# Kernel optimization log

Hardware: AMD Instinct MI355X
Metric: run time of the kernel (lower is better)

## Reference

```python
import jax, jax.numpy as jnp
import numpy as np

IN_FEATURES = 4096
OUT_FEATURES = 11008
GROUP_SIZE = 32
M_TOKENS = 32
Q_MID = 8  # int4 midpoint: dequant = (q - 8) * scale + zero


def setup_inputs() -> dict:
    key = jax.random.key(0)
    k1, k2, k3, k4 = jax.random.split(key, 4)
    n_groups = IN_FEATURES // GROUP_SIZE
    inputs = {
        "input": jax.random.normal(k1, (M_TOKENS, IN_FEATURES), dtype=jnp.float32),
        "weight": jax.random.randint(k2, (OUT_FEATURES, IN_FEATURES), 0, 16, dtype=jnp.int32),
        "scales_and_zeros": jax.random.normal(k3, (n_groups, OUT_FEATURES, 2), dtype=jnp.float32),
        "bias": jax.random.normal(k4, (OUT_FEATURES,), dtype=jnp.float32),
        "group_size": GROUP_SIZE,
    }
    return inputs


def reference(input, weight, scales_and_zeros, bias, group_size):
    out_features, in_features = weight.shape
    n_groups = in_features // group_size
    # scales/zeros per (group, out) -> [out, n_groups]
    scale = scales_and_zeros[..., 0].T  # [out, G]
    zero = scales_and_zeros[..., 1].T   # [out, G]
    # dequantize int4 weight: w = (q - 8) * scale + zero, per group along in_features
    q = weight.astype(jnp.float32).reshape(out_features, n_groups, group_size)
    w_fp = (q - Q_MID) * scale[:, :, None] + zero[:, :, None]  # [out, G, gs]
    w_fp = w_fp.reshape(out_features, in_features)
    # y = x @ W^T + b
    y = jnp.einsum("bi,oi->bo", input, w_fp) + bias
    return y
```

## Files before the change

kernel.cpp:

```cpp
#include <hip/hip_runtime.h>
#include <hip/hip_bf16.h>
#include <stdint.h>

#define M_TOK 32
#define IN_F 4096
#define OUT_F 11008
#define NSPLIT 8
#define KRANGE (IN_F / NSPLIT)
#define NSTEP  (KRANGE / 32)
#define NKK    (IN_F / 32)
#define NBUF   4

typedef __attribute__((ext_vector_type(8))) short bf16x8;
typedef __attribute__((ext_vector_type(4))) float f32x4;

__device__ inline uint32_t pack_bf16(float a, float b) {
    __hip_bfloat16 ha = __float2bfloat16(a);
    __hip_bfloat16 hb = __float2bfloat16(b);
    uint16_t ua = *(uint16_t*)&ha;
    uint16_t ub = *(uint16_t*)&hb;
    return (uint32_t)ua | ((uint32_t)ub << 16);
}

__global__ void init_out_kernel(const float* __restrict__ bias, float* __restrict__ out) {
    int o = blockIdx.x * 256 + threadIdx.x;
    int m = blockIdx.y;
    out[(size_t)m * OUT_F + o] = bias[o];
}

__global__ void prepack_a_kernel(const float* __restrict__ x, uint4* __restrict__ ws4) {
    int u  = blockIdx.x * 256 + threadIdx.x;
    int kk = u >> 6;
    int l  = u & 63;
    int lm = l & 15;
    int lq = l >> 4;
    int kb = kk * 32 + lq * 8;
    #pragma unroll
    for (int j = 0; j < 2; ++j) {
        const float* xp = x + (size_t)(lm + 16 * j) * IN_F + kb;
        union { uint4 q; uint32_t u[4]; } f;
        f.u[0] = pack_bf16(xp[0], xp[1]);
        f.u[1] = pack_bf16(xp[2], xp[3]);
        f.u[2] = pack_bf16(xp[4], xp[5]);
        f.u[3] = pack_bf16(xp[6], xp[7]);
        ws4[(size_t)kk * 128 + j * 64 + l] = f.q;
    }
}

__launch_bounds__(256)
__global__ void qgemm_kernel(const uint4* __restrict__ af,
                             const int* __restrict__ wq,
                             const float* __restrict__ sz,
                             float* __restrict__ out) {
    __shared__ int    lds_w[NBUF][64 * 32];
    __shared__ uint4  lds_a[NSTEP * 128];
    __shared__ float2 lds_s[NSTEP * 64];

    const int bid = blockIdx.x;
    const int ks  = bid & (NSPLIT - 1);
    const int nb  = bid >> 3;
    const int t   = threadIdx.x;
    const int wv  = t >> 6;
    const int l   = t & 63;
    const int lm  = l & 15;
    const int lq  = l >> 4;

    const int row0 = nb * 64;
    const int row  = row0 + wv * 16 + lm;
    const int k0   = ks * KRANGE;

    const int rs    = t >> 3;
    const int cs    = t & 7;
    const int* gw0  = wq + (size_t)(row0 + rs) * IN_F + k0 + ((cs ^ (rs & 7)) * 4);
    const int* gw1  = gw0 + (size_t)32 * IN_F;

#define GLL(src, dst) \
    __builtin_amdgcn_global_load_lds( \
        (const __attribute__((address_space(1))) int*)(src), \
        (__attribute__((address_space(3))) int*)(dst), 16, 0, 0)

#define STAGE(buf, tile) do {                                 \
    GLL(gw0 + (tile) * 32, &lds_w[(buf)][wv * 256]);          \
    GLL(gw1 + (tile) * 32, &lds_w[(buf)][1024 + wv * 256]);   \
} while (0)

#define WAITV(N) do {                                         \
    asm volatile("s_waitcnt vmcnt(" #N ")" ::: "memory");     \
    __builtin_amdgcn_sched_barrier(0);                        \
} while (0)

#define BAR() do {                                            \
    __builtin_amdgcn_s_barrier();                             \
    __builtin_amdgcn_sched_barrier(0);                        \
} while (0)

    const int rloc = wv * 16 + lm;
    const int c0   = rloc * 32 + (((2 * lq)     ^ (rloc & 7)) * 4);
    const int c1   = rloc * 32 + (((2 * lq + 1) ^ (rloc & 7)) * 4);

    {
        const uint4* asrc = af + (size_t)ks * (NSTEP * 128) + t;
        #pragma unroll
        for (int i = 0; i < 8; ++i)
            GLL(asrc + i * 256, &lds_a[i * 256 + wv * 64]);
    }
    {
        const float* szsrc = sz + ((size_t)(k0 >> 5) * OUT_F + row0) * 2
                                + (size_t)(t >> 5) * OUT_F * 2 + (t & 31) * 4;
        GLL(szsrc,                        &lds_s[wv * 128]);
        GLL(szsrc + (size_t)8 * OUT_F * 2, &lds_s[512 + wv * 128]);
    }
    STAGE(0, 0);
    STAGE(1, 1);
    STAGE(2, 2);
    __builtin_amdgcn_sched_barrier(0);

    f32x4 acc0 = {0.f, 0.f, 0.f, 0.f};
    f32x4 acc1 = {0.f, 0.f, 0.f, 0.f};

#define STEP_BODY(cb, st) do {                                                  \
    int4   q0 = *(const int4*)(&lds_w[(cb)][c0]);                               \
    int4   q1 = *(const int4*)(&lds_w[(cb)][c1]);                               \
    union { uint4 q; bf16x8 v; } a0, a1;                                        \
    a0.q = lds_a[(st) * 128 + l];                                               \
    a1.q = lds_a[(st) * 128 + 64 + l];                                          \
    float2 sv = lds_s[(st) * 64 + rloc];                                        \
    const float sc = sv.x;                                                      \
    const float zp = sv.y - 8.0f * sv.x;                                        \
    union { bf16x8 v; uint32_t u[4]; } bf;                                      \
    bf.u[0] = pack_bf16((float)q0.x * sc + zp, (float)q0.y * sc + zp);          \
    bf.u[1] = pack_bf16((float)q0.z * sc + zp, (float)q0.w * sc + zp);          \
    bf.u[2] = pack_bf16((float)q1.x * sc + zp, (float)q1.y * sc + zp);          \
    bf.u[3] = pack_bf16((float)q1.z * sc + zp, (float)q1.w * sc + zp);          \
    acc0 = __builtin_amdgcn_mfma_f32_16x16x32_bf16(a0.v, bf.v, acc0, 0, 0, 0);  \
    acc1 = __builtin_amdgcn_mfma_f32_16x16x32_bf16(a1.v, bf.v, acc1, 0, 0, 0);  \
} while (0)

    #pragma unroll 4
    for (int s = 0; s < 12; ++s) {
        WAITV(4);
        BAR();
        STAGE((s + 3) & 3, s + 3);
        STEP_BODY(s & 3, s);
    }
    WAITV(4); BAR(); STAGE(3, 15); STEP_BODY(0, 12);
    WAITV(4); BAR(); STEP_BODY(1, 13);
    WAITV(2); BAR(); STEP_BODY(2, 14);
    WAITV(0); BAR(); STEP_BODY(3, 15);

#undef STEP_BODY
#undef STAGE
#undef GLL
#undef WAITV
#undef BAR

    const int ocol = row;
    #pragma unroll
    for (int i = 0; i < 4; ++i) {
        int m0 = lq * 4 + i;
        atomicAdd(&out[(size_t)m0 * OUT_F + ocol], acc0[i]);
        atomicAdd(&out[(size_t)(16 + m0) * OUT_F + ocol], acc1[i]);
    }
}

extern "C" void kernel_launch(void* const* d_in, const int* in_sizes, int n_in,
                              void* d_out, int out_size, void* d_ws, size_t ws_size,
                              hipStream_t stream) {
    const float* x    = (const float*)d_in[0];
    const int*   wq   = (const int*)d_in[1];
    const float* sz   = (const float*)d_in[2];
    const float* bias = (const float*)d_in[3];
    float* out = (float*)d_out;
    uint4* af  = (uint4*)d_ws;

    prepack_a_kernel<<<dim3(NKK * 64 / 256), 256, 0, stream>>>(x, af);

    dim3 gi(OUT_F / 256, M_TOK);
    init_out_kernel<<<gi, 256, 0, stream>>>(bias, out);

    dim3 gg((OUT_F / 64) * NSPLIT);
    qgemm_kernel<<<gg, 256, 0, stream>>>((const uint4*)af, wq, sz, out);
}
```

Measured before the change: 265.8 us.

## Reduce split-K to 2 and make each wave pipeline its own weight tiles barrier-free

Split-K drops from 8 to 2, so each block walks 64 K-steps instead of 16, which cuts the number of fp32 atomic adds into the output. Each wave now stages only its own 16 weight rows into LDS, so the block-wide barriers are removed. Activation fragments and scales/zeros are loaded straight into registers per step instead of being bulk-staged in LDS. The cost is fewer blocks (344 instead of 1376), so there is less parallelism across CUs, plus more register pressure and more vmcnt-tracked loads per step.

Result: slower. 275.2 us (+3.5%).

```diff
diff --git a/kernel.cpp b/kernel.cpp
--- a/kernel.cpp
+++ b/kernel.cpp
@@ -5,11 +5,10 @@
 #define M_TOK 32
 #define IN_F 4096
 #define OUT_F 11008
-#define NSPLIT 8
+#define NSPLIT 2
 #define KRANGE (IN_F / NSPLIT)
-#define NSTEP  (KRANGE / 32)
+#define NST    (KRANGE / 32)
 #define NKK    (IN_F / 32)
-#define NBUF   4
 
 typedef __attribute__((ext_vector_type(8))) short bf16x8;
 typedef __attribute__((ext_vector_type(4))) float f32x4;
@@ -52,13 +51,11 @@
                              const int* __restrict__ wq,
                              const float* __restrict__ sz,
                              float* __restrict__ out) {
-    __shared__ int    lds_w[NBUF][64 * 32];
-    __shared__ uint4  lds_a[NSTEP * 128];
-    __shared__ float2 lds_s[NSTEP * 64];
+    __shared__ int lds_w[4][2048];
 
     const int bid = blockIdx.x;
     const int ks  = bid & (NSPLIT - 1);
-    const int nb  = bid >> 3;
+    const int nb  = bid >> 1;
     const int t   = threadIdx.x;
     const int wv  = t >> 6;
     const int l   = t & 63;
@@ -69,90 +66,82 @@
     const int row  = row0 + wv * 16 + lm;
     const int k0   = ks * KRANGE;
 
-    const int rs    = t >> 3;
-    const int cs    = t & 7;
-    const int* gw0  = wq + (size_t)(row0 + rs) * IN_F + k0 + ((cs ^ (rs & 7)) * 4);
-    const int* gw1  = gw0 + (size_t)32 * IN_F;
+    const int rr   = l >> 3;
+    const int cc   = l & 7;
+    const int* gwa = wq + (size_t)(row0 + wv * 16 + rr) * IN_F + k0 + ((cc ^ rr) * 4);
+    const int* gwb = gwa + (size_t)8 * IN_F;
+
+    const int c0 = wv * 512 + lm * 32 + (((2 * lq)     ^ (lm & 7)) * 4);
+    const int c1 = wv * 512 + lm * 32 + (((2 * lq + 1) ^ (lm & 7)) * 4);
+
+    const uint4* ap  = af + (size_t)(ks * NST) * 128 + l;
+    const float* szp = sz + ((size_t)(ks * NST) * OUT_F + row) * 2;
 
 #define GLL(src, dst) \
     __builtin_amdgcn_global_load_lds( \
         (const __attribute__((address_space(1))) int*)(src), \
         (__attribute__((address_space(3))) int*)(dst), 16, 0, 0)
 
-#define STAGE(buf, tile) do {                                 \
-    GLL(gw0 + (tile) * 32, &lds_w[(buf)][wv * 256]);          \
-    GLL(gw1 + (tile) * 32, &lds_w[(buf)][1024 + wv * 256]);   \
-} while (0)
-
 #define WAITV(N) do {                                         \
     asm volatile("s_waitcnt vmcnt(" #N ")" ::: "memory");     \
     __builtin_amdgcn_sched_barrier(0);                        \
 } while (0)
 
-#define BAR() do {                                            \
-    __builtin_amdgcn_s_barrier();                             \
-    __builtin_amdgcn_sched_barrier(0);                        \
+    uint4  A0_0, A0_1, A0_2, A0_3;
+    uint4  A1_0, A1_1, A1_2, A1_3;
+    float2 S_0,  S_1,  S_2,  S_3;
+
+#define PREFETCH(slot, stepexpr) do {                                   \
+    const int _s = (stepexpr);                                          \
+    GLL(gwa + (size_t)_s * 32, &lds_w[slot][wv * 512]);                 \
+    GLL(gwb + (size_t)_s * 32, &lds_w[slot][wv * 512 + 256]);           \
+    A0_##slot = ap[(size_t)_s * 128];                                   \
+    A1_##slot = ap[(size_t)_s * 128 + 64];                              \
+    S_##slot  = *(const float2*)(szp + (size_t)_s * OUT_F * 2);         \
 } while (0)
-
-    const int rloc = wv * 16 + lm;
-    const int c0   = rloc * 32 + (((2 * lq)     ^ (rloc & 7)) * 4);
-    const int c1   = rloc * 32 + (((2 * lq + 1) ^ (rloc & 7)) * 4);
-
-    {
-        const uint4* asrc = af + (size_t)ks * (NSTEP * 128) + t;
-        #pragma unroll
-        for (int i = 0; i < 8; ++i)
-            GLL(asrc + i * 256, &lds_a[i * 256 + wv * 64]);
-    }
-    {
-        const float* szsrc = sz + ((size_t)(k0 >> 5) * OUT_F + row0) * 2
-                                + (size_t)(t >> 5) * OUT_F * 2 + (t & 31) * 4;
-        GLL(szsrc,                        &lds_s[wv * 128]);
-        GLL(szsrc + (size_t)8 * OUT_F * 2, &lds_s[512 + wv * 128]);
-    }
-    STAGE(0, 0);
-    STAGE(1, 1);
-    STAGE(2, 2);
-    __builtin_amdgcn_sched_barrier(0);
 
     f32x4 acc0 = {0.f, 0.f, 0.f, 0.f};
     f32x4 acc1 = {0.f, 0.f, 0.f, 0.f};
 
-#define STEP_BODY(cb, st) do {                                                  \
-    int4   q0 = *(const int4*)(&lds_w[(cb)][c0]);                               \
-    int4   q1 = *(const int4*)(&lds_w[(cb)][c1]);                               \
-    union { uint4 q; bf16x8 v; } a0, a1;                                        \
-    a0.q = lds_a[(st) * 128 + l];                                               \
-    a1.q = lds_a[(st) * 128 + 64 + l];                                          \
-    float2 sv = lds_s[(st) * 64 + rloc];                                        \
-    const float sc = sv.x;                                                      \
-    const float zp = sv.y - 8.0f * sv.x;                                        \
+#define COMPUTE(slot) do {                                                      \
+    int4 q0 = *(const int4*)(&lds_w[slot][c0]);                                 \
+    int4 q1 = *(const int4*)(&lds_w[slot][c1]);                                 \
+    const float sc = S_##slot.x;                                                \
+    const float zp = S_##slot.y - 8.0f * sc;                                    \
+    union { uint4 q; bf16x8 v; } ua, ub;                                        \
+    ua.q = A0_##slot;                                                           \
+    ub.q = A1_##slot;                                                           \
     union { bf16x8 v; uint32_t u[4]; } bf;                                      \
     bf.u[0] = pack_bf16((float)q0.x * sc + zp, (float)q0.y * sc + zp);          \
     bf.u[1] = pack_bf16((float)q0.z * sc + zp, (float)q0.w * sc + zp);          \
     bf.u[2] = pack_bf16((float)q1.x * sc + zp, (float)q1.y * sc + zp);          \
     bf.u[3] = pack_bf16((float)q1.z * sc + zp, (float)q1.w * sc + zp);          \
-    acc0 = __builtin_amdgcn_mfma_f32_16x16x32_bf16(a0.v, bf.v, acc0, 0, 0, 0);  \
-    acc1 = __builtin_amdgcn_mfma_f32_16x16x32_bf16(a1.v, bf.v, acc1, 0, 0, 0);  \
+    acc0 = __builtin_amdgcn_mfma_f32_16x16x32_bf16(ua.v, bf.v, acc0, 0, 0, 0);  \
+    acc1 = __builtin_amdgcn_mfma_f32_16x16x32_bf16(ub.v, bf.v, acc1, 0, 0, 0);  \
 } while (0)
 
-    #pragma unroll 4
-    for (int s = 0; s < 12; ++s) {
-        WAITV(4);
-        BAR();
-        STAGE((s + 3) & 3, s + 3);
-        STEP_BODY(s & 3, s);
+    PREFETCH(0, 0);
+    PREFETCH(1, 1);
+    PREFETCH(2, 2);
+    __builtin_amdgcn_sched_barrier(0);
+
+    #pragma unroll 1
+    for (int u = 0; u < 15; ++u) {
+        const int sb = u * 4;
+        WAITV(10); PREFETCH(3, sb + 3); COMPUTE(0);
+        WAITV(10); PREFETCH(0, sb + 4); COMPUTE(1);
+        WAITV(10); PREFETCH(1, sb + 5); COMPUTE(2);
+        WAITV(10); PREFETCH(2, sb + 6); COMPUTE(3);
     }
-    WAITV(4); BAR(); STAGE(3, 15); STEP_BODY(0, 12);
-    WAITV(4); BAR(); STEP_BODY(1, 13);
-    WAITV(2); BAR(); STEP_BODY(2, 14);
-    WAITV(0); BAR(); STEP_BODY(3, 15);
+    WAITV(10); PREFETCH(3, 63); COMPUTE(0);
+    WAITV(10); COMPUTE(1);
+    WAITV(5);  COMPUTE(2);
+    WAITV(0);  COMPUTE(3);
 
-#undef STEP_BODY
-#undef STAGE
+#undef COMPUTE
+#undef PREFETCH
 #undef GLL
 #undef WAITV
-#undef BAR
 
     const int ocol = row;
     #pragma unroll
```
